# Kernel tuning notes

Hardware: AMD Instinct MI355X
Metric: run time of the kernel (lower is better)

## Reference

```python
import jax, jax.numpy as jnp
import numpy as np

B, N, D, E, H = 8, 256, 128, 32, 4
HD = D // H
EPS = 1e-5


def setup_inputs() -> dict:
    key = jax.random.key(0)
    ks = jax.random.split(key, 20)
    idx = jnp.arange(N)

    h = jax.random.normal(ks[0], (B, N, D), dtype=jnp.float32)
    adj = (jax.random.uniform(ks[1], (B, N, N)) < 0.5).astype(jnp.float32)
    adj = adj.at[:, idx, idx].set(1.0)
    edge_features = jax.random.normal(ks[2], (B, N, N, E), dtype=jnp.float32)
    src_mask = (jax.random.uniform(ks[3], (B, N, N)) < 0.7).astype(jnp.float32)
    src_mask = src_mask.at[:, idx, idx].set(1.0)

    s = 1.0 / np.sqrt(D)
    se = 1.0 / np.sqrt(E)
    p = {
        "gcn_w": jax.random.normal(ks[4], (D, D)) * s,
        "gcn_b": jnp.zeros((D,)),
        "edge_w": jax.random.normal(ks[5], (D, E)) * se,
        "edge_b": jnp.zeros((D,)),
        "wq": jax.random.normal(ks[6], (D, D)) * s,
        "wk": jax.random.normal(ks[7], (D, D)) * s,
        "wv": jax.random.normal(ks[8], (D, D)) * s,
        "bq": jnp.zeros((D,)),
        "bk": jnp.zeros((D,)),
        "bv": jnp.zeros((D,)),
        "out_w": jax.random.normal(ks[9], (D, D)) * s,
        "out_b": jnp.zeros((D,)),
        "ln_g": jnp.ones((D,)),
        "ln_b": jnp.zeros((D,)),
    }
    return {"h": h, "adj": adj, "edge_features": edge_features, "src_mask": src_mask, **p}


def reference(h, adj, edge_features, src_mask,
              gcn_w, gcn_b, edge_w, edge_b,
              wq, wk, wv, bq, bk, bv, out_w, out_b, ln_g, ln_b):
    b, n, d = h.shape

    # --- GCN branch: degree-normalized aggregation with self-loops ---
    adj_sl = adj + jnp.eye(n, dtype=h.dtype)[None]          # (B,N,N)
    deg = adj_sl.sum(-1, keepdims=True)                      # (B,N,1)
    h_agg = jnp.einsum('bnm,bmd->bnd', adj_sl, h) / deg
    h_gcn = h_agg @ gcn_w.T + gcn_b                          # (B,N,D)

    # --- edge-conditioned key/value: h_ij = h_j + edge_emb ---
    edge_emb = jnp.einsum('bnme,de->bnmd', edge_features, edge_w) + edge_b
    h_ij = h[:, None, :, :] + edge_emb                       # (B,N,N,D)

    # key padding mask: True where edge absent (masked)
    masked = (adj * src_mask) == 0                           # (B,N,N)

    # --- multi-head attention, one query per node ---
    q = (h @ wq.T + bq).reshape(b, n, H, HD)                 # (B,N,H,HD)
    k = (jnp.einsum('bnmd,ed->bnme', h_ij, wk) + bk).reshape(b, n, n, H, HD)
    v = (jnp.einsum('bnmd,ed->bnme', h_ij, wv) + bv).reshape(b, n, n, H, HD)

    scores = jnp.einsum('bnhd,bnmhd->bnhm', q, k) / np.sqrt(HD)  # (B,N,H,N)
    scores = jnp.where(masked[:, :, None, :], -jnp.inf, scores)
    attn = jax.nn.softmax(scores, axis=-1)
    o = jnp.einsum('bnhm,bnmhd->bnhd', attn, v).reshape(b, n, d)
    o = o @ out_w.T + out_b                                  # (B,N,D)

    # residual + layernorm (dropout is identity in eval)
    x = h + o
    mu = x.mean(-1, keepdims=True)
    var = ((x - mu) ** 2).mean(-1, keepdims=True)
    h_attn = ln_g * (x - mu) / jnp.sqrt(var + EPS) + ln_b

    return h_gcn + h_attn
```

## Files before the change

### kernel.cpp

```cpp
#include <hip/hip_runtime.h>
#include <hip/hip_bf16.h>

#define OFF_WQT 0
#define OFF_WKT 16384
#define OFF_WVT 32768
#define OFF_OWT 49152
#define OFF_GWT 65536
#define OFF_WKE 81920
#define OFF_WVET 86016
#define OFF_KB  90112
#define OFF_VB  90240
#define OFF_SC  90368
#define OFF_QSP 98560
#define OFF_QEP 229632
#define OFF_HG  360704
#define OFF_K0P 622848
#define OFF_V0P 753920

using half2_t = __attribute__((ext_vector_type(2))) __fp16;

static __device__ __forceinline__ half2_t u2h(unsigned int u){
  union { unsigned int u; half2_t h; } x; x.u = u; return x.h;
}
static __device__ __forceinline__ unsigned int pkf16(float a, float b){
  union { half2_t h; unsigned int u; } x;
  x.h = __builtin_amdgcn_cvt_pkrtz(a, b);
  return x.u;
}
static __device__ __forceinline__ float fdot2(unsigned int a, unsigned int b, float c){
  return __builtin_amdgcn_fdot2(u2h(a), u2h(b), c, false);
}

__global__ __launch_bounds__(256) void prep_kernel(
    const float* __restrict__ wq, const float* __restrict__ wk,
    const float* __restrict__ wv, const float* __restrict__ out_w,
    const float* __restrict__ gcn_w, const float* __restrict__ edge_w,
    const float* __restrict__ edge_b, const float* __restrict__ bk,
    const float* __restrict__ bv, float* __restrict__ ws)
{
  int blk = blockIdx.x, t = threadIdx.x;
  if (blk < 320) {
    int w = blk >> 6;
    int e0 = (blk & 63) * 256 + t;
    const float* src = (w==0) ? wq : (w==1) ? wk : (w==2) ? wv : (w==3) ? out_w : gcn_w;
    float* dst = ws + ((w==0) ? OFF_WQT : (w==1) ? OFF_WKT : (w==2) ? OFF_WVT
                      : (w==3) ? OFF_OWT : OFF_GWT);
    int k = e0 >> 7, d = e0 & 127;
    dst[e0] = src[d*128 + k];
  } else if (blk < 352) {
    int idx = blk - 320;
    int which = idx >> 4;
    int e0 = (idx & 15) * 256 + t;
    int dd = e0 >> 5, e = e0 & 31;
    const float* W = which ? wv : wk;
    float acc = 0.f;
    #pragma unroll 4
    for (int k2 = 0; k2 < 128; ++k2) acc += W[dd*128+k2] * edge_w[k2*32+e];
    if (which) ws[OFF_WVET + e*128 + dd] = acc;
    else       ws[OFF_WKE + e0] = acc;
  } else {
    int dd = t & 127;
    const float* W  = (t < 128) ? wk : wv;
    const float* bb = (t < 128) ? bk : bv;
    float acc = bb[dd];
    #pragma unroll 4
    for (int k2 = 0; k2 < 128; ++k2) acc += W[dd*128+k2] * edge_b[k2];
    ws[((t < 128) ? OFF_KB : OFF_VB) + dd] = acc;
  }
}

__global__ __launch_bounds__(256) void proj_kernel(
    const float* __restrict__ h, const float* __restrict__ adj,
    const float* __restrict__ bq, const float* __restrict__ gcn_b,
    float* __restrict__ ws)
{
  __shared__ float h_lds[256];
  __shared__ float adj_lds[512];
  __shared__ float p1[2][2][128];
  __shared__ float p2[2][2][128];
  __shared__ float p3[2][2][128];
  __shared__ float qrow[2*132];
  __shared__ float qe_l[2*132];
  __shared__ float dpart[2][2];
  __shared__ float ha_lds[2*132];

  int t = threadIdx.x;
  int d = t & 127, kh = t >> 7;
  int r0 = blockIdx.x * 2;
  int b  = r0 >> 8, n0 = r0 & 255;
  unsigned int* wsu = (unsigned int*)ws;

  if (t < 64)  ((float4*)h_lds)[t]   = ((const float4*)(h   + (size_t)r0*128))[t];
  if (t < 128) ((float4*)adj_lds)[t] = ((const float4*)(adj + (size_t)r0*256))[t];
  __syncthreads();

  {
    const float* wqT = ws + OFF_WQT;
    const float* wkT = ws + OFF_WKT;
    const float* wvT = ws + OFF_WVT;
    float aq0=0,aq1=0,ak0=0,ak1=0,av0=0,av1=0;
    #pragma unroll 4
    for (int kk = 0; kk < 64; ++kk) {
      int k = kh*64 + kk;
      float qw = wqT[k*128+d], kw = wkT[k*128+d], vw = wvT[k*128+d];
      float h0 = h_lds[k], h1 = h_lds[128+k];
      aq0 += qw*h0; aq1 += qw*h1;
      ak0 += kw*h0; ak1 += kw*h1;
      av0 += vw*h0; av1 += vw*h1;
    }
    p1[kh][0][d]=aq0; p1[kh][1][d]=aq1;
    p2[kh][0][d]=ak0; p2[kh][1][d]=ak1;
    p3[kh][0][d]=av0; p3[kh][1][d]=av1;
  }
  __syncthreads();

  {
    int i = t >> 7, dd = t & 127;
    const float inv = 0.17677669529663687f;
    qrow[i*132 + dd] = (p1[0][i][dd] + p1[1][i][dd] + bq[dd]) * inv;
  }
  {
    int i = (t >> 6) & 1, pr = t & 63;
    if (t < 128) {
      float k0 = p2[0][i][2*pr] + p2[1][i][2*pr];
      float k1 = p2[0][i][2*pr+1] + p2[1][i][2*pr+1];
      wsu[OFF_K0P + (size_t)(r0+i)*64 + pr] = pkf16(k0, k1);
    } else {
      float v0 = p3[0][i][2*pr] + p3[1][i][2*pr];
      float v1 = p3[0][i][2*pr+1] + p3[1][i][2*pr+1];
      wsu[OFF_V0P + (size_t)(r0+i)*64 + pr] = pkf16(v0, v1);
    }
  }
  __syncthreads();

  if (t < 128) {
    int i = t >> 6, pr = t & 63;
    wsu[OFF_QSP + (size_t)(r0+i)*64 + pr] = pkf16(qrow[i*132 + 2*pr], qrow[i*132 + 2*pr+1]);
  }
  {
    int i = t >> 7, he = t & 127, hh = he >> 5, e = he & 31;
    float acc = 0.f;
    #pragma unroll
    for (int j = 0; j < 32; ++j)
      acc += ws[OFF_WKE + (hh*32 + j)*32 + e] * qrow[i*132 + hh*32 + j];
    qe_l[i*132 + he] = acc;
  }
  if (t < 8) {
    int i = t >> 2, hh = t & 3;
    float acc = 0.f;
    #pragma unroll
    for (int j = 0; j < 32; ++j)
      acc += qrow[i*132 + hh*32 + j] * ws[OFF_KB + hh*32 + j];
    ws[OFF_SC + (size_t)(r0+i)*4 + hh] = acc;
  }
  {
    float ag0=0, ag1=0, dg0=0, dg1=0;
    #pragma unroll 4
    for (int mm = 0; mm < 128; ++mm) {
      int ml = kh*128 + mm;
      float hv = h[((size_t)b*256 + ml)*128 + d];
      float a0 = adj_lds[ml]       + ((ml == n0)     ? 1.0f : 0.0f);
      float a1 = adj_lds[256 + ml] + ((ml == n0 + 1) ? 1.0f : 0.0f);
      ag0 += a0*hv; ag1 += a1*hv; dg0 += a0; dg1 += a1;
    }
    p1[kh][0][d]=ag0; p1[kh][1][d]=ag1;
    if (d == 0) { dpart[kh][0]=dg0; dpart[kh][1]=dg1; }
  }
  __syncthreads();

  if (t < 128) {
    int i = t >> 6, pr = t & 63;
    wsu[OFF_QEP + (size_t)(r0+i)*64 + pr] = pkf16(qe_l[i*132 + 2*pr], qe_l[i*132 + 2*pr+1]);
  }
  {
    int i = t >> 7, dd = t & 127;
    ha_lds[i*132 + dd] = (p1[0][i][dd] + p1[1][i][dd]) / (dpart[0][i] + dpart[1][i]);
  }
  __syncthreads();

  {
    const float* gwT = ws + OFF_GWT;
    float g0=0, g1=0;
    #pragma unroll 4
    for (int kk = 0; kk < 64; ++kk) {
      int k = kh*64 + kk;
      float gw = gwT[k*128+d];
      g0 += gw * ha_lds[k];
      g1 += gw * ha_lds[132 + k];
    }
    p2[kh][0][d]=g0; p2[kh][1][d]=g1;
  }
  __syncthreads();
  {
    int i = t >> 7, dd = t & 127;
    ws[OFF_HG + (size_t)(r0+i)*128 + dd] = p2[0][i][dd] + p2[1][i][dd] + gcn_b[dd];
  }
}

__global__ __launch_bounds__(256) void attn_kernel(
    const float* __restrict__ edge, const float* __restrict__ adj,
    const float* __restrict__ srcm, const float* __restrict__ h,
    const float* __restrict__ out_b, const float* __restrict__ ln_g,
    const float* __restrict__ ln_b, const float* __restrict__ ws,
    float* __restrict__ out)
{
  __shared__ unsigned int e_buf[3*64*18];
  __shared__ unsigned int q_lds[128];
  __shared__ float s_chunk[2][4*66];
  __shared__ float wpart[16];
  __shared__ float ovh[128];
  __shared__ float eb_l[128];
  __shared__ float ov_l[128];
  __shared__ float o_l[128];
  __shared__ float px[256];
  __shared__ float stat[4];

  const int t  = threadIdx.x;
  const int bn = blockIdx.x;
  const int b  = bn >> 8;
  const int hh = t & 3;
  const int mq = t >> 2;
  const unsigned int* wsu = (const unsigned int*)ws;

  const float4* et = (const float4*)(edge + (size_t)bn*8192);

  float4 va = et[t];
  float4 vb = et[256 + t];
  float mp0 = adj[(size_t)bn*256 +       mq] * srcm[(size_t)bn*256 +       mq];
  float mp1 = adj[(size_t)bn*256 +  64 + mq] * srcm[(size_t)bn*256 +  64 + mq];
  float mp2 = adj[(size_t)bn*256 + 128 + mq] * srcm[(size_t)bn*256 + 128 + mq];
  float mp3 = adj[(size_t)bn*256 + 192 + mq] * srcm[(size_t)bn*256 + 192 + mq];

  if (t < 64)       q_lds[t] = wsu[OFF_QSP + (size_t)bn*64 + t];
  else if (t < 128) q_lds[t] = wsu[OFF_QEP + (size_t)bn*64 + (t - 64)];

  float sconst = ws[OFF_SC + (size_t)bn*4 + hh];
  const unsigned int* K0 = wsu + OFF_K0P + (size_t)b*256*64;

  float h_pre = 0.f, hg_pre = 0.f;
  if (t < 128) {
    h_pre  = h[(size_t)bn*128 + t];
    hg_pre = ws[OFF_HG + (size_t)bn*128 + t];
  }

  {
    int lr = t >> 3, c4 = t & 7;
    uint2 pk;
    pk.x = pkf16(va.x, va.y); pk.y = pkf16(va.z, va.w);
    *(uint2*)(e_buf + lr*18 + c4*2) = pk;
    uint2 pk2;
    pk2.x = pkf16(vb.x, vb.y); pk2.y = pkf16(vb.z, vb.w);
    *(uint2*)(e_buf + (32 + lr)*18 + c4*2) = pk2;
  }
  va = et[512 + t];
  vb = et[768 + t];
  __syncthreads();

  float exacc = 0.f;
  float acc4 = 0.f;
  float acc5x = 0.f, acc5y = 0.f;

  #pragma unroll
  for (int c = 0; c < 4; ++c) {
    const unsigned int* ebc = e_buf + (c % 3)*64*18;

    {
      int gm = c*64 + mq;
      float acc = sconst;
      const uint4* kr4 = (const uint4*)(K0 + (size_t)gm*64 + hh*16);
      const uint4* qs4 = (const uint4*)(q_lds + hh*16);
      const uint4* qe4 = (const uint4*)(q_lds + 64 + hh*16);
      #pragma unroll
      for (int j4 = 0; j4 < 4; ++j4) {
        uint4 kw = kr4[j4];
        uint4 qw = qs4[j4];
        acc = fdot2(qw.x, kw.x, acc);
        acc = fdot2(qw.y, kw.y, acc);
        acc = fdot2(qw.z, kw.z, acc);
        acc = fdot2(qw.w, kw.w, acc);
      }
      const uint2* er = (const uint2*)(ebc + mq*18);
      #pragma unroll
      for (int j4 = 0; j4 < 4; ++j4) {
        uint4 qw = qe4[j4];
        uint2 w0 = er[2*j4], w1 = er[2*j4+1];
        acc = fdot2(qw.x, w0.x, acc);
        acc = fdot2(qw.y, w0.y, acc);
        acc = fdot2(qw.z, w1.x, acc);
        acc = fdot2(qw.w, w1.y, acc);
      }
      float mp = (c==0) ? mp0 : (c==1) ? mp1 : (c==2) ? mp2 : mp3;
      float ex = (mp == 0.0f) ? 0.0f : __expf(acc);
      s_chunk[c & 1][hh*66 + mq] = ex;
      exacc += ex;
    }

    if (c > 0) {
      const unsigned int* ebp = e_buf + ((c-1) % 3)*64*18;
      const float* scp = s_chunk[(c-1) & 1];
      if (t < 128) {
        int e = t & 31, ht = t >> 5;
        const float* sc_ = scp + ht*66;
        const unsigned int* ebr = ebp + (e >> 1);
        bool hi = (e & 1);
        float a0 = 0.f, a1 = 0.f;
        #pragma unroll 8
        for (int m = 0; m < 64; m += 2) {
          float s0 = sc_[m], s1 = sc_[m+1];
          half2_t w0 = u2h(ebr[m*18]);
          half2_t w1 = u2h(ebr[(m+1)*18]);
          float e0 = hi ? (float)w0.y : (float)w0.x;
          float e1 = hi ? (float)w1.y : (float)w1.x;
          a0 += s0*e0; a1 += s1*e1;
        }
        acc4 += a0 + a1;
      } else {
        int idx = t - 128;
        int j = idx & 63, mh = idx >> 6;
        int head = j >> 4;
        const float* sc_ = scp + head*66 + mh*32;
        const unsigned int* vp = wsu + OFF_V0P + ((size_t)b*256 + (c-1)*64 + mh*32)*64 + j;
        float a0 = 0.f, a1 = 0.f;
        #pragma unroll 8
        for (int m = 0; m < 32; ++m) {
          float s = sc_[m];
          half2_t v = u2h(vp[(size_t)m*64]);
          a0 += s*(float)v.x; a1 += s*(float)v.y;
        }
        acc5x += a0; acc5y += a1;
      }
    }

    if (c < 3) {
      unsigned int* ebn = e_buf + ((c+1) % 3)*64*18;
      int lr = t >> 3, c4 = t & 7;
      uint2 pk;
      pk.x = pkf16(va.x, va.y); pk.y = pkf16(va.z, va.w);
      *(uint2*)(ebn + lr*18 + c4*2) = pk;
      uint2 pk2;
      pk2.x = pkf16(vb.x, vb.y); pk2.y = pkf16(vb.z, vb.w);
      *(uint2*)(ebn + (32 + lr)*18 + c4*2) = pk2;
      if (c < 2) {
        va = et[(c+2)*512 + t];
        vb = et[(c+2)*512 + 256 + t];
      }
    }
    __syncthreads();
  }

  exacc += __shfl_down(exacc, 4);
  exacc += __shfl_down(exacc, 8);
  exacc += __shfl_down(exacc, 16);
  exacc += __shfl_down(exacc, 32);
  if ((t & 63) < 4) wpart[(t >> 6)*4 + hh] = exacc;

  {
    const unsigned int* ebp = e_buf + (3 % 3)*64*18;
    const float* scp = s_chunk[1];
    if (t < 128) {
      int e = t & 31, ht = t >> 5;
      const float* sc_ = scp + ht*66;
      const unsigned int* ebr = ebp + (e >> 1);
      bool hi = (e & 1);
      float a0 = 0.f, a1 = 0.f;
      #pragma unroll 8
      for (int m = 0; m < 64; m += 2) {
        float s0 = sc_[m], s1 = sc_[m+1];
        half2_t w0 = u2h(ebr[m*18]);
        half2_t w1 = u2h(ebr[(m+1)*18]);
        float e0 = hi ? (float)w0.y : (float)w0.x;
        float e1 = hi ? (float)w1.y : (float)w1.x;
        a0 += s0*e0; a1 += s1*e1;
      }
      acc4 += a0 + a1;
    } else {
      int idx = t - 128;
      int j = idx & 63, mh = idx >> 6;
      int head = j >> 4;
      const float* sc_ = scp + head*66 + mh*32;
      const unsigned int* vp = wsu + OFF_V0P + ((size_t)b*256 + 192 + mh*32)*64 + j;
      float a0 = 0.f, a1 = 0.f;
      #pragma unroll 8
      for (int m = 0; m < 32; ++m) {
        float s = sc_[m];
        half2_t v = u2h(vp[(size_t)m*64]);
        a0 += s*(float)v.x; a1 += s*(float)v.y;
      }
      acc5x += a0; acc5y += a1;
    }
  }
  if (t >= 192) {
    int j = (t - 128) & 63;
    float2 p; p.x = acc5x; p.y = acc5y;
    *(float2*)(ovh + j*2) = p;
  }
  __syncthreads();

  if (t < 128) {
    int ht = t >> 5;
    float inv = 1.0f / (wpart[ht] + wpart[4+ht] + wpart[8+ht] + wpart[12+ht]);
    eb_l[t] = acc4 * inv;
  } else if (t < 192) {
    int j = t - 128, head = j >> 4;
    float inv = 1.0f / (wpart[head] + wpart[4+head] + wpart[8+head] + wpart[12+head]);
    float2 oh = *(const float2*)(ovh + j*2);
    float2 res;
    res.x = (acc5x + oh.x)*inv + ws[OFF_VB + 2*j];
    res.y = (acc5y + oh.y)*inv + ws[OFF_VB + 2*j + 1];
    *(float2*)(ov_l + 2*j) = res;
  }
  __syncthreads();

  if (t < 128) {
    int hd = t >> 5;
    float acc = ov_l[t];
    const float* wveT = ws + OFF_WVET;
    #pragma unroll 8
    for (int e = 0; e < 32; ++e) acc += wveT[e*128 + t] * eb_l[hd*32 + e];
    o_l[t] = acc;
  }
  __syncthreads();

  {
    int d = t & 127, kh = t >> 7;
    const float* owT = ws + OFF_OWT;
    float xa = 0.f;
    #pragma unroll 8
    for (int kk = 0; kk < 64; ++kk) {
      int k = kh*64 + kk;
      xa += owT[k*128 + d] * o_l[k];
    }
    px[kh*128 + d] = xa;
  }
  __syncthreads();

  float x = 0.f;
  if (t < 128) {
    x = px[t] + px[128 + t] + out_b[t] + h_pre;
    float s = x, ss = x*x;
    #pragma unroll
    for (int off = 32; off > 0; off >>= 1) {
      s  += __shfl_down(s,  off);
      ss += __shfl_down(ss, off);
    }
    if ((t & 63) == 0) { stat[t >> 6] = s; stat[2 + (t >> 6)] = ss; }
  }
  __syncthreads();

  if (t < 128) {
    float mu   = (stat[0] + stat[1]) * (1.0f/128.0f);
    float var  = (stat[2] + stat[3]) * (1.0f/128.0f) - mu*mu;
    float rstd = rsqrtf(var + 1e-5f);
    out[(size_t)bn*128 + t] =
        ln_g[t]*(x - mu)*rstd + ln_b[t] + hg_pre;
  }
}

extern "C" void kernel_launch(void* const* d_in, const int* in_sizes, int n_in,
                              void* d_out, int out_size, void* d_ws, size_t ws_size,
                              hipStream_t stream) {
  (void)in_sizes; (void)n_in; (void)out_size; (void)ws_size;
  const float* h     = (const float*)d_in[0];
  const float* adj   = (const float*)d_in[1];
  const float* edge  = (const float*)d_in[2];
  const float* srcm  = (const float*)d_in[3];
  const float* gcn_w = (const float*)d_in[4];
  const float* gcn_b = (const float*)d_in[5];
  const float* edge_w= (const float*)d_in[6];
  const float* edge_b= (const float*)d_in[7];
  const float* wq    = (const float*)d_in[8];
  const float* wk    = (const float*)d_in[9];
  const float* wv    = (const float*)d_in[10];
  const float* bq    = (const float*)d_in[11];
  const float* bk    = (const float*)d_in[12];
  const float* bv    = (const float*)d_in[13];
  const float* out_w = (const float*)d_in[14];
  const float* out_b = (const float*)d_in[15];
  const float* ln_g  = (const float*)d_in[16];
  const float* ln_b  = (const float*)d_in[17];

  float* ws  = (float*)d_ws;
  float* out = (float*)d_out;

  prep_kernel<<<353, 256, 0, stream>>>(wq, wk, wv, out_w, gcn_w, edge_w, edge_b, bk, bv, ws);
  proj_kernel<<<1024, 256, 0, stream>>>(h, adj, bq, gcn_b, ws);
  attn_kernel<<<2048, 256, 0, stream>>>(edge, adj, srcm, h, out_b, ln_g, ln_b, ws, out);
}
```

Baseline: 184.0 us.

## Read edge features directly from global memory instead of staging fp16 in LDS

Drops the triple-buffered LDS staging of edge features, where the data was packed to fp16 and prefetched one chunk ahead. The score and the edge-weighted aggregation now read fp32 edge values straight from global memory and compute in fp32 FMA. The q edge-part is unpacked once into fp32 LDS. This removes the LDS writes, packing work and the prefetch pipeline. In exchange, each element is read from global or cache twice, the per-thread row loads are not coalesced, and the latency that the prefetch used to hide is now exposed.

```diff
diff --git a/kernel.cpp b/kernel.cpp
--- a/kernel.cpp
+++ b/kernel.cpp
@@ -204,8 +204,8 @@
     const float* __restrict__ ln_b, const float* __restrict__ ws,
     float* __restrict__ out)
 {
-  __shared__ unsigned int e_buf[3*64*18];
-  __shared__ unsigned int q_lds[128];
+  __shared__ unsigned int q_lds[64];
+  __shared__ float qe_lds[128];
   __shared__ float s_chunk[2][4*66];
   __shared__ float wpart[16];
   __shared__ float ovh[128];
@@ -222,17 +222,24 @@
   const int mq = t >> 2;
   const unsigned int* wsu = (const unsigned int*)ws;
 
-  const float4* et = (const float4*)(edge + (size_t)bn*8192);
-
-  float4 va = et[t];
-  float4 vb = et[256 + t];
+  const float* eg = edge + (size_t)bn*8192;
+  const float4* et = (const float4*)eg;
+
   float mp0 = adj[(size_t)bn*256 +       mq] * srcm[(size_t)bn*256 +       mq];
   float mp1 = adj[(size_t)bn*256 +  64 + mq] * srcm[(size_t)bn*256 +  64 + mq];
   float mp2 = adj[(size_t)bn*256 + 128 + mq] * srcm[(size_t)bn*256 + 128 + mq];
   float mp3 = adj[(size_t)bn*256 + 192 + mq] * srcm[(size_t)bn*256 + 192 + mq];
 
-  if (t < 64)       q_lds[t] = wsu[OFF_QSP + (size_t)bn*64 + t];
-  else if (t < 128) q_lds[t] = wsu[OFF_QEP + (size_t)bn*64 + (t - 64)];
+  if (t < 64) {
+    q_lds[t] = wsu[OFF_QSP + (size_t)bn*64 + t];
+  } else if (t < 128) {
+    int idx = t - 64;
+    unsigned int w = wsu[OFF_QEP + (size_t)bn*64 + idx];
+    half2_t hv = u2h(w);
+    int head = idx >> 4, j = idx & 15;
+    qe_lds[head*32 + 2*j]     = (float)hv.x;
+    qe_lds[head*32 + 2*j + 1] = (float)hv.y;
+  }
 
   float sconst = ws[OFF_SC + (size_t)bn*4 + hh];
   const unsigned int* K0 = wsu + OFF_K0P + (size_t)b*256*64;
@@ -242,18 +249,6 @@
     h_pre  = h[(size_t)bn*128 + t];
     hg_pre = ws[OFF_HG + (size_t)bn*128 + t];
   }
-
-  {
-    int lr = t >> 3, c4 = t & 7;
-    uint2 pk;
-    pk.x = pkf16(va.x, va.y); pk.y = pkf16(va.z, va.w);
-    *(uint2*)(e_buf + lr*18 + c4*2) = pk;
-    uint2 pk2;
-    pk2.x = pkf16(vb.x, vb.y); pk2.y = pkf16(vb.z, vb.w);
-    *(uint2*)(e_buf + (32 + lr)*18 + c4*2) = pk2;
-  }
-  va = et[512 + t];
-  vb = et[768 + t];
   __syncthreads();
 
   float exacc = 0.f;
@@ -262,14 +257,11 @@
 
   #pragma unroll
   for (int c = 0; c < 4; ++c) {
-    const unsigned int* ebc = e_buf + (c % 3)*64*18;
-
     {
       int gm = c*64 + mq;
       float acc = sconst;
       const uint4* kr4 = (const uint4*)(K0 + (size_t)gm*64 + hh*16);
       const uint4* qs4 = (const uint4*)(q_lds + hh*16);
-      const uint4* qe4 = (const uint4*)(q_lds + 64 + hh*16);
       #pragma unroll
       for (int j4 = 0; j4 < 4; ++j4) {
         uint4 kw = kr4[j4];
@@ -279,15 +271,15 @@
         acc = fdot2(qw.z, kw.z, acc);
         acc = fdot2(qw.w, kw.w, acc);
       }
-      const uint2* er = (const uint2*)(ebc + mq*18);
+      const float4* erow = et + (size_t)gm*8;
+      const float* qe = qe_lds + hh*32;
       #pragma unroll
-      for (int j4 = 0; j4 < 4; ++j4) {
-        uint4 qw = qe4[j4];
-        uint2 w0 = er[2*j4], w1 = er[2*j4+1];
-        acc = fdot2(qw.x, w0.x, acc);
-        acc = fdot2(qw.y, w0.y, acc);
-        acc = fdot2(qw.z, w1.x, acc);
-        acc = fdot2(qw.w, w1.y, acc);
+      for (int j = 0; j < 8; ++j) {
+        float4 v = erow[j];
+        acc = fmaf(qe[4*j+0], v.x, acc);
+        acc = fmaf(qe[4*j+1], v.y, acc);
+        acc = fmaf(qe[4*j+2], v.z, acc);
+        acc = fmaf(qe[4*j+3], v.w, acc);
       }
       float mp = (c==0) ? mp0 : (c==1) ? mp1 : (c==2) ? mp2 : mp3;
       float ex = (mp == 0.0f) ? 0.0f : __expf(acc);
@@ -296,22 +288,16 @@
     }
 
     if (c > 0) {
-      const unsigned int* ebp = e_buf + ((c-1) % 3)*64*18;
       const float* scp = s_chunk[(c-1) & 1];
       if (t < 128) {
         int e = t & 31, ht = t >> 5;
         const float* sc_ = scp + ht*66;
-        const unsigned int* ebr = ebp + (e >> 1);
-        bool hi = (e & 1);
+        const float* ecol = eg + ((size_t)(c-1)*64)*32 + e;
         float a0 = 0.f, a1 = 0.f;
         #pragma unroll 8
         for (int m = 0; m < 64; m += 2) {
-          float s0 = sc_[m], s1 = sc_[m+1];
-          half2_t w0 = u2h(ebr[m*18]);
-          half2_t w1 = u2h(ebr[(m+1)*18]);
-          float e0 = hi ? (float)w0.y : (float)w0.x;
-          float e1 = hi ? (float)w1.y : (float)w1.x;
-          a0 += s0*e0; a1 += s1*e1;
+          a0 = fmaf(sc_[m],   ecol[(size_t)m*32],     a0);
+          a1 = fmaf(sc_[m+1], ecol[(size_t)(m+1)*32], a1);
         }
         acc4 += a0 + a1;
       } else {
@@ -330,21 +316,6 @@
         acc5x += a0; acc5y += a1;
       }
     }
-
-    if (c < 3) {
-      unsigned int* ebn = e_buf + ((c+1) % 3)*64*18;
-      int lr = t >> 3, c4 = t & 7;
-      uint2 pk;
-      pk.x = pkf16(va.x, va.y); pk.y = pkf16(va.z, va.w);
-      *(uint2*)(ebn + lr*18 + c4*2) = pk;
-      uint2 pk2;
-      pk2.x = pkf16(vb.x, vb.y); pk2.y = pkf16(vb.z, vb.w);
-      *(uint2*)(ebn + (32 + lr)*18 + c4*2) = pk2;
-      if (c < 2) {
-        va = et[(c+2)*512 + t];
-        vb = et[(c+2)*512 + 256 + t];
-      }
-    }
     __syncthreads();
   }
 
@@ -355,22 +326,16 @@
   if ((t & 63) < 4) wpart[(t >> 6)*4 + hh] = exacc;
 
   {
-    const unsigned int* ebp = e_buf + (3 % 3)*64*18;
     const float* scp = s_chunk[1];
     if (t < 128) {
       int e = t & 31, ht = t >> 5;
       const float* sc_ = scp + ht*66;
-      const unsigned int* ebr = ebp + (e >> 1);
-      bool hi = (e & 1);
+      const float* ecol = eg + (size_t)192*32 + e;
       float a0 = 0.f, a1 = 0.f;
       #pragma unroll 8
       for (int m = 0; m < 64; m += 2) {
-        float s0 = sc_[m], s1 = sc_[m+1];
-        half2_t w0 = u2h(ebr[m*18]);
-        half2_t w1 = u2h(ebr[(m+1)*18]);
-        float e0 = hi ? (float)w0.y : (float)w0.x;
-        float e1 = hi ? (float)w1.y : (float)w1.x;
-        a0 += s0*e0; a1 += s1*e1;
+        a0 = fmaf(sc_[m],   ecol[(size_t)m*32],     a0);
+        a1 = fmaf(sc_[m+1], ecol[(size_t)(m+1)*32], a1);
       }
       acc4 += a0 + a1;
     } else {
```

Result: slower. 195.9 us (+6.5%).
